# Performance work log

Hardware: AMD Instinct MI355X
Metric: run time of the kernel (lower is better)

## Reference

```python
import jax, jax.numpy as jnp
import numpy as np

B, L, H, P, S = 16, 2048, 1024, 16, 128
PAR_LEN, SENT_LEN = L // P, L // S  # 128, 16


def setup_inputs() -> dict:
    key = jax.random.key(0)
    k1, k2, k3 = jax.random.split(key, 3)
    backbone_outputs = jax.random.normal(k1, (B, L, H), dtype=jnp.float32)
    attention_mask = jnp.ones((B, L), dtype=jnp.int64)
    # structured ragged offsets: paragraph p spans [p*128, p*128+127],
    # sentence s starts at s*16 -> every paragraph contains 8 sentence heads
    par_head = jnp.tile(jnp.arange(P, dtype=jnp.int64)[None, :] * PAR_LEN, (B, 1))
    par_tail = par_head + (PAR_LEN - 1)
    sent_head = jnp.tile(jnp.arange(S, dtype=jnp.int64)[None, :] * SENT_LEN, (B, 1))
    sent_tail = sent_head + (SENT_LEN - 1)
    paragraph_attention_mask = jnp.ones((B, P), dtype=jnp.int64)
    sentence_attention_mask = jnp.ones((B, S), dtype=jnp.int64)
    # classifier params: Linear(H, 5)
    W = jax.random.normal(k2, (5, H), dtype=jnp.float32) / np.sqrt(H)
    b = jax.random.normal(k3, (5,), dtype=jnp.float32) * 0.01
    return {
        "backbone_outputs": backbone_outputs,
        "attention_mask": attention_mask,
        "paragraph_head_idxs": par_head,
        "paragraph_tail_idxs": par_tail,
        "paragraph_attention_mask": paragraph_attention_mask,
        "sentence_head_idxs": sent_head,
        "sentence_tail_idxs": sent_tail,
        "sentence_attention_mask": sentence_attention_mask,
        "W": W,
        "b": b,
    }


def reference(backbone_outputs, attention_mask, paragraph_head_idxs,
              paragraph_tail_idxs, paragraph_attention_mask,
              sentence_head_idxs, sentence_tail_idxs,
              sentence_attention_mask, W, b):
    # gather sentence-head token embeddings: [B, S, H]
    emb = jnp.take_along_axis(backbone_outputs, sentence_head_idxs[:, :, None], axis=1)
    sh = sentence_head_idxs[:, None, :]  # [B, 1, S]
    # membership: sentence head lies inside paragraph [head, tail]
    sel = (paragraph_head_idxs[:, :, None] <= sh) & (sh <= paragraph_tail_idxs[:, :, None])  # [B,P,S]
    self_f = sel.astype(emb.dtype)
    sent_cnt = jnp.maximum(self_f.sum(-1), 1.0)  # [B, P]
    # sentence -> paragraph mean (level 1)
    par_rep = jnp.einsum('bps,bsh->bph', self_f, emb) / sent_cnt[..., None]
    # paragraph skipped if tail-head<=2 or selected_head_idxs.any() is False
    par_valid = ((paragraph_tail_idxs - paragraph_head_idxs) > 2) & jnp.any(sel & (sh != 0), axis=-1)
    pv = par_valid.astype(emb.dtype)  # [B, P]
    par_cnt = jnp.maximum(pv.sum(-1), 1.0)
    # paragraph -> essay mean (level 2)
    final = jnp.einsum('bp,bph->bh', pv, par_rep) / par_cnt[:, None]
    return final @ W.T + b  # [B, 5]
```

## Files before the change

### kernel.cpp

```cpp
#include <hip/hip_runtime.h>

#define B_ 16
#define L_ 2048
#define H_ 1024
#define P_ 16
#define S_ 128

__global__ void __launch_bounds__(1024) msh_fused(
        const float* __restrict__ backbone,
        const int* __restrict__ par_head,
        const int* __restrict__ par_tail,
        const int* __restrict__ sent_head,
        const float* __restrict__ W,
        const float* __restrict__ bias,
        float* __restrict__ out) {
    int b = blockIdx.x;
    int t = threadIdx.x;

    __shared__ int   sh[S_];
    __shared__ int   ph[P_], pt[P_];
    __shared__ float inv_scnt[P_];
    __shared__ int   validp[P_];
    __shared__ float invpar;
    __shared__ float wgt[S_];
    __shared__ float red[16][5];

    if (t < S_) sh[t] = sent_head[b * S_ + t];
    if (t >= S_ && t < S_ + P_) {
        int p = t - S_;
        ph[p] = par_head[b * P_ + p];
        pt[p] = par_tail[b * P_ + p];
    }
    __syncthreads();

    {
        int p = t >> 6, lane = t & 63;
        int h0 = ph[p], t0 = pt[p];
        int s1 = lane, s2 = lane + 64;
        int in1 = (h0 <= sh[s1]) && (sh[s1] <= t0);
        int in2 = (h0 <= sh[s2]) && (sh[s2] <= t0);
        int cnt = in1 + in2;
        int nz  = (in1 && sh[s1] != 0) || (in2 && sh[s2] != 0);
        for (int off = 32; off > 0; off >>= 1) {
            cnt += __shfl_down(cnt, off, 64);
            nz  |= __shfl_down(nz,  off, 64);
        }
        if (lane == 0) {
            int valid = ((t0 - h0) > 2) && nz;
            validp[p] = valid;
            inv_scnt[p] = valid ? 1.0f / (float)(cnt > 1 ? cnt : 1) : 0.0f;
        }
    }
    __syncthreads();
    if (t == 0) {
        int pc = 0;
        for (int p = 0; p < P_; ++p) pc += validp[p];
        invpar = 1.0f / (float)(pc > 1 ? pc : 1);
    }
    __syncthreads();
    if (t < S_) {
        int myh = sh[t];
        float w = 0.0f;
        for (int p = 0; p < P_; ++p)
            if (ph[p] <= myh && myh <= pt[p]) w += inv_scnt[p];
        wgt[t] = w * invpar;
    }
    __syncthreads();

    int grp = t >> 8, q = t & 255;
    const float4* bb4 = reinterpret_cast<const float4*>(
        backbone + (size_t)b * L_ * H_);
    float4 acc = make_float4(0.f, 0.f, 0.f, 0.f);
#pragma unroll 4
    for (int s = grp; s < S_; s += 4) {
        int row = sh[s];
        float w = wgt[s];
        float4 v = bb4[row * (H_ / 4) + q];
        acc.x += w * v.x; acc.y += w * v.y; acc.z += w * v.z; acc.w += w * v.w;
    }

    const float4* W4 = reinterpret_cast<const float4*>(W);
    float pj[5];
#pragma unroll
    for (int j = 0; j < 5; ++j) {
        float4 wv = W4[j * (H_ / 4) + q];
        pj[j] = acc.x * wv.x + acc.y * wv.y + acc.z * wv.z + acc.w * wv.w;
    }
    int wave = t >> 6, lane = t & 63;
#pragma unroll
    for (int j = 0; j < 5; ++j) {
        float v = pj[j];
        for (int off = 32; off > 0; off >>= 1) v += __shfl_down(v, off, 64);
        pj[j] = v;
    }
    if (lane == 0) {
#pragma unroll
        for (int j = 0; j < 5; ++j) red[wave][j] = pj[j];
    }
    __syncthreads();

    if (t < 5) {
        float tot = 0.0f;
#pragma unroll
        for (int i = 0; i < 16; ++i) tot += red[i][t];
        out[b * 5 + t] = tot + bias[t];
    }
}

extern "C" void kernel_launch(void* const* d_in, const int* in_sizes, int n_in,
                              void* d_out, int out_size, void* d_ws, size_t ws_size,
                              hipStream_t stream) {
    const float* backbone  = (const float*)d_in[0];
    const int*   par_head  = (const int*)d_in[2];
    const int*   par_tail  = (const int*)d_in[3];
    const int*   sent_head = (const int*)d_in[5];
    const float* W         = (const float*)d_in[8];
    const float* bias      = (const float*)d_in[9];

    float* out = (float*)d_out;

    msh_fused<<<B_, 1024, 0, stream>>>(backbone, par_head, par_tail, sent_head,
                                       W, bias, out);
}
```

Baseline: 13.48 us.

## Split into weight-init kernel and wide gather kernel with atomic accumulation

The single 16-block fused kernel becomes two kernels. A small init kernel computes per-sentence weights into workspace and seeds the output with the bias. A main kernel then spreads the weighted gather and projection over 256 blocks, each covering 8 sentences, and accumulates partial results with atomicAdd. This puts far more blocks on the GPU for the memory-bound gather and skips rows whose weight is zero. The cost is a second launch, a global round trip for the weights, and float atomics that make the summation order nondeterministic.

```diff
diff --git a/kernel.cpp b/kernel.cpp
--- a/kernel.cpp
+++ b/kernel.cpp
@@ -6,49 +6,44 @@
 #define P_ 16
 #define S_ 128
 
-__global__ void __launch_bounds__(1024) msh_fused(
-        const float* __restrict__ backbone,
+__global__ void __launch_bounds__(128) msh_init(
         const int* __restrict__ par_head,
         const int* __restrict__ par_tail,
         const int* __restrict__ sent_head,
-        const float* __restrict__ W,
         const float* __restrict__ bias,
+        float* __restrict__ w_out,
         float* __restrict__ out) {
     int b = blockIdx.x;
     int t = threadIdx.x;
 
     __shared__ int   sh[S_];
-    __shared__ int   ph[P_], pt[P_];
     __shared__ float inv_scnt[P_];
     __shared__ int   validp[P_];
     __shared__ float invpar;
-    __shared__ float wgt[S_];
-    __shared__ float red[16][5];
 
-    if (t < S_) sh[t] = sent_head[b * S_ + t];
-    if (t >= S_ && t < S_ + P_) {
-        int p = t - S_;
-        ph[p] = par_head[b * P_ + p];
-        pt[p] = par_tail[b * P_ + p];
-    }
+    sh[t] = sent_head[b * S_ + t];
     __syncthreads();
 
     {
-        int p = t >> 6, lane = t & 63;
-        int h0 = ph[p], t0 = pt[p];
-        int s1 = lane, s2 = lane + 64;
-        int in1 = (h0 <= sh[s1]) && (sh[s1] <= t0);
-        int in2 = (h0 <= sh[s2]) && (sh[s2] <= t0);
-        int cnt = in1 + in2;
-        int nz  = (in1 && sh[s1] != 0) || (in2 && sh[s2] != 0);
-        for (int off = 32; off > 0; off >>= 1) {
-            cnt += __shfl_down(cnt, off, 64);
-            nz  |= __shfl_down(nz,  off, 64);
-        }
-        if (lane == 0) {
-            int valid = ((t0 - h0) > 2) && nz;
-            validp[p] = valid;
-            inv_scnt[p] = valid ? 1.0f / (float)(cnt > 1 ? cnt : 1) : 0.0f;
+        int wave = t >> 6, lane = t & 63;
+        for (int k = 0; k < 8; ++k) {
+            int p = wave * 8 + k;
+            int h0 = par_head[b * P_ + p];
+            int t0 = par_tail[b * P_ + p];
+            int s1 = lane, s2 = lane + 64;
+            int in1 = (h0 <= sh[s1]) && (sh[s1] <= t0);
+            int in2 = (h0 <= sh[s2]) && (sh[s2] <= t0);
+            int cnt = in1 + in2;
+            int nz  = (in1 && sh[s1] != 0) || (in2 && sh[s2] != 0);
+            for (int off = 32; off > 0; off >>= 1) {
+                cnt += __shfl_down(cnt, off, 64);
+                nz  |= __shfl_down(nz,  off, 64);
+            }
+            if (lane == 0) {
+                int valid = ((t0 - h0) > 2) && nz;
+                validp[p] = valid;
+                inv_scnt[p] = valid ? 1.0f / (float)(cnt > 1 ? cnt : 1) : 0.0f;
+            }
         }
     }
     __syncthreads();
@@ -58,34 +53,55 @@
         invpar = 1.0f / (float)(pc > 1 ? pc : 1);
     }
     __syncthreads();
-    if (t < S_) {
-        int myh = sh[t];
-        float w = 0.0f;
-        for (int p = 0; p < P_; ++p)
-            if (ph[p] <= myh && myh <= pt[p]) w += inv_scnt[p];
-        wgt[t] = w * invpar;
+
+    int myh = sh[t];
+    float w = 0.0f;
+    for (int p = 0; p < P_; ++p) {
+        int h0 = par_head[b * P_ + p];
+        int t0 = par_tail[b * P_ + p];
+        if (h0 <= myh && myh <= t0) w += inv_scnt[p];
     }
-    __syncthreads();
+    w_out[b * S_ + t] = w * invpar;
 
-    int grp = t >> 8, q = t & 255;
+    if (t < 5) out[b * 5 + t] = bias[t];
+}
+
+__global__ void __launch_bounds__(256) msh_main(
+        const float* __restrict__ backbone,
+        const int* __restrict__ sent_head,
+        const float* __restrict__ W,
+        const float* __restrict__ wgt,
+        float* __restrict__ out) {
+    int blk = blockIdx.x;
+    int b   = blk >> 4;
+    int sub = blk & 15;
+    int t   = threadIdx.x;
+
     const float4* bb4 = reinterpret_cast<const float4*>(
         backbone + (size_t)b * L_ * H_);
+
     float4 acc = make_float4(0.f, 0.f, 0.f, 0.f);
-#pragma unroll 4
-    for (int s = grp; s < S_; s += 4) {
-        int row = sh[s];
-        float w = wgt[s];
-        float4 v = bb4[row * (H_ / 4) + q];
-        acc.x += w * v.x; acc.y += w * v.y; acc.z += w * v.z; acc.w += w * v.w;
+    int s0 = sub * 8;
+#pragma unroll
+    for (int i = 0; i < 8; ++i) {
+        int s = s0 + i;
+        float w = wgt[b * S_ + s];
+        if (w != 0.0f) {
+            int row = sent_head[b * S_ + s];
+            float4 v = bb4[(size_t)row * (H_ / 4) + t];
+            acc.x += w * v.x; acc.y += w * v.y;
+            acc.z += w * v.z; acc.w += w * v.w;
+        }
     }
 
     const float4* W4 = reinterpret_cast<const float4*>(W);
     float pj[5];
 #pragma unroll
     for (int j = 0; j < 5; ++j) {
-        float4 wv = W4[j * (H_ / 4) + q];
+        float4 wv = W4[j * (H_ / 4) + t];
         pj[j] = acc.x * wv.x + acc.y * wv.y + acc.z * wv.z + acc.w * wv.w;
     }
+
     int wave = t >> 6, lane = t & 63;
 #pragma unroll
     for (int j = 0; j < 5; ++j) {
@@ -93,6 +109,8 @@
         for (int off = 32; off > 0; off >>= 1) v += __shfl_down(v, off, 64);
         pj[j] = v;
     }
+
+    __shared__ float red[4][5];
     if (lane == 0) {
 #pragma unroll
         for (int j = 0; j < 5; ++j) red[wave][j] = pj[j];
@@ -100,10 +118,8 @@
     __syncthreads();
 
     if (t < 5) {
-        float tot = 0.0f;
-#pragma unroll
-        for (int i = 0; i < 16; ++i) tot += red[i][t];
-        out[b * 5 + t] = tot + bias[t];
+        float tot = red[0][t] + red[1][t] + red[2][t] + red[3][t];
+        atomicAdd(out + b * 5 + t, tot);
     }
 }
 
@@ -117,8 +133,9 @@
     const float* W         = (const float*)d_in[8];
     const float* bias      = (const float*)d_in[9];
 
-    float* out = (float*)d_out;
+    float* out  = (float*)d_out;
+    float* w_ws = (float*)d_ws;
 
-    msh_fused<<<B_, 1024, 0, stream>>>(backbone, par_head, par_tail, sent_head,
-                                       W, bias, out);
+    msh_init<<<B_, 128, 0, stream>>>(par_head, par_tail, sent_head, bias, w_ws, out);
+    msh_main<<<B_ * 16, 256, 0, stream>>>(backbone, sent_head, W, w_ws, out);
 }
```

Measured after the change: 16.71 us. 1.24x slower.

## Prefetch backbone rows and W before weight computation, drop a barrier

Applied to the files above, without the earlier changes.

Issues the first eight gathered backbone row loads and the five W row loads right after the index loads, before the paragraph-weight computation. Their global-memory latency then overlaps the shared-memory weight setup. The valid-paragraph count is now computed redundantly by each of the first 128 threads, which removes one single-thread phase and one barrier. The cost is higher register pressure from holding 13 float4 values in a 1024-thread block.

```diff
diff --git a/kernel.cpp b/kernel.cpp
--- a/kernel.cpp
+++ b/kernel.cpp
@@ -16,25 +16,39 @@
         float* __restrict__ out) {
     int b = blockIdx.x;
     int t = threadIdx.x;
+    int wave = t >> 6, lane = t & 63;
+    int grp = t >> 8, q = t & 255;
 
     __shared__ int   sh[S_];
     __shared__ int   ph[P_], pt[P_];
     __shared__ float inv_scnt[P_];
     __shared__ int   validp[P_];
-    __shared__ float invpar;
     __shared__ float wgt[S_];
     __shared__ float red[16][5];
 
     if (t < S_) sh[t] = sent_head[b * S_ + t];
-    if (t >= S_ && t < S_ + P_) {
-        int p = t - S_;
-        ph[p] = par_head[b * P_ + p];
-        pt[p] = par_tail[b * P_ + p];
-    }
+    if (t < P_) { ph[t] = par_head[b * P_ + t]; pt[t] = par_tail[b * P_ + t]; }
     __syncthreads();
 
+    const float4* bb4 = reinterpret_cast<const float4*>(
+        backbone + (size_t)b * L_ * H_);
+    float4 v0 = bb4[(size_t)sh[grp +  0] * (H_/4) + q];
+    float4 v1 = bb4[(size_t)sh[grp +  4] * (H_/4) + q];
+    float4 v2 = bb4[(size_t)sh[grp +  8] * (H_/4) + q];
+    float4 v3 = bb4[(size_t)sh[grp + 12] * (H_/4) + q];
+    float4 v4 = bb4[(size_t)sh[grp + 16] * (H_/4) + q];
+    float4 v5 = bb4[(size_t)sh[grp + 20] * (H_/4) + q];
+    float4 v6 = bb4[(size_t)sh[grp + 24] * (H_/4) + q];
+    float4 v7 = bb4[(size_t)sh[grp + 28] * (H_/4) + q];
+    const float4* W4 = reinterpret_cast<const float4*>(W);
+    float4 wj0 = W4[0 * (H_/4) + q];
+    float4 wj1 = W4[1 * (H_/4) + q];
+    float4 wj2 = W4[2 * (H_/4) + q];
+    float4 wj3 = W4[3 * (H_/4) + q];
+    float4 wj4 = W4[4 * (H_/4) + q];
+
     {
-        int p = t >> 6, lane = t & 63;
+        int p  = wave;
         int h0 = ph[p], t0 = pt[p];
         int s1 = lane, s2 = lane + 64;
         int in1 = (h0 <= sh[s1]) && (sh[s1] <= t0);
@@ -52,41 +66,43 @@
         }
     }
     __syncthreads();
-    if (t == 0) {
-        int pc = 0;
-        for (int p = 0; p < P_; ++p) pc += validp[p];
-        invpar = 1.0f / (float)(pc > 1 ? pc : 1);
-    }
-    __syncthreads();
     if (t < S_) {
         int myh = sh[t];
-        float w = 0.0f;
-        for (int p = 0; p < P_; ++p)
+        float w = 0.0f; int pc = 0;
+        for (int p = 0; p < P_; ++p) {
+            pc += validp[p];
             if (ph[p] <= myh && myh <= pt[p]) w += inv_scnt[p];
-        wgt[t] = w * invpar;
+        }
+        wgt[t] = w / (float)(pc > 1 ? pc : 1);
     }
     __syncthreads();
 
-    int grp = t >> 8, q = t & 255;
-    const float4* bb4 = reinterpret_cast<const float4*>(
-        backbone + (size_t)b * L_ * H_);
     float4 acc = make_float4(0.f, 0.f, 0.f, 0.f);
-#pragma unroll 4
-    for (int s = grp; s < S_; s += 4) {
-        int row = sh[s];
+#define FMA4(wv, v) do { float _w = (wv); \
+        acc.x += _w * (v).x; acc.y += _w * (v).y; \
+        acc.z += _w * (v).z; acc.w += _w * (v).w; } while (0)
+    FMA4(wgt[grp +  0], v0);
+    FMA4(wgt[grp +  4], v1);
+    FMA4(wgt[grp +  8], v2);
+    FMA4(wgt[grp + 12], v3);
+    FMA4(wgt[grp + 16], v4);
+    FMA4(wgt[grp + 20], v5);
+    FMA4(wgt[grp + 24], v6);
+    FMA4(wgt[grp + 28], v7);
+#pragma unroll 8
+    for (int s = grp + 32; s < S_; s += 4) {
         float w = wgt[s];
-        float4 v = bb4[row * (H_ / 4) + q];
-        acc.x += w * v.x; acc.y += w * v.y; acc.z += w * v.z; acc.w += w * v.w;
+        float4 v = bb4[(size_t)sh[s] * (H_/4) + q];
+        FMA4(w, v);
     }
+#undef FMA4
 
-    const float4* W4 = reinterpret_cast<const float4*>(W);
     float pj[5];
-#pragma unroll
-    for (int j = 0; j < 5; ++j) {
-        float4 wv = W4[j * (H_ / 4) + q];
-        pj[j] = acc.x * wv.x + acc.y * wv.y + acc.z * wv.z + acc.w * wv.w;
-    }
-    int wave = t >> 6, lane = t & 63;
+    pj[0] = acc.x*wj0.x + acc.y*wj0.y + acc.z*wj0.z + acc.w*wj0.w;
+    pj[1] = acc.x*wj1.x + acc.y*wj1.y + acc.z*wj1.z + acc.w*wj1.w;
+    pj[2] = acc.x*wj2.x + acc.y*wj2.y + acc.z*wj2.z + acc.w*wj2.w;
+    pj[3] = acc.x*wj3.x + acc.y*wj3.y + acc.z*wj3.z + acc.w*wj3.w;
+    pj[4] = acc.x*wj4.x + acc.y*wj4.y + acc.z*wj4.z + acc.w*wj4.w;
 #pragma unroll
     for (int j = 0; j < 5; ++j) {
         float v = pj[j];
```

Result: faster. 12.37 us (-8.2%).

## Issue all backbone and W row loads before computing sentence weights

Applied to the files above, without the earlier changes.

All 32 gathered backbone float4 rows per thread, plus the classifier weights, are now loaded into registers right after the index loads, before the paragraph-validity and weight computation. This lets the global-memory latency overlap with the shared-memory bookkeeping instead of starting only after it. One barrier and the single-thread paragraph-count step are removed by having each weight thread count valid paragraphs itself. It needs about 150 VGPRs per thread for the preloaded data, which at 1024 threads per block risks register pressure or spilling.

```diff
diff --git a/kernel.cpp b/kernel.cpp
--- a/kernel.cpp
+++ b/kernel.cpp
@@ -16,25 +16,35 @@
         float* __restrict__ out) {
     int b = blockIdx.x;
     int t = threadIdx.x;
+    int wave = t >> 6, lane = t & 63;
+    int grp = t >> 8, q = t & 255;
 
     __shared__ int   sh[S_];
     __shared__ int   ph[P_], pt[P_];
     __shared__ float inv_scnt[P_];
     __shared__ int   validp[P_];
-    __shared__ float invpar;
     __shared__ float wgt[S_];
     __shared__ float red[16][5];
 
     if (t < S_) sh[t] = sent_head[b * S_ + t];
-    if (t >= S_ && t < S_ + P_) {
-        int p = t - S_;
-        ph[p] = par_head[b * P_ + p];
-        pt[p] = par_tail[b * P_ + p];
-    }
+    if (t < P_) { ph[t] = par_head[b * P_ + t]; pt[t] = par_tail[b * P_ + t]; }
     __syncthreads();
 
+    const float4* bb4 = reinterpret_cast<const float4*>(
+        backbone + (size_t)b * L_ * H_);
+    float4 v[32];
+#pragma unroll
+    for (int i = 0; i < 32; ++i)
+        v[i] = bb4[(size_t)sh[grp + 4 * i] * (H_ / 4) + q];
+
+    const float4* W4 = reinterpret_cast<const float4*>(W);
+    float4 wj[5];
+#pragma unroll
+    for (int j = 0; j < 5; ++j)
+        wj[j] = W4[j * (H_ / 4) + q];
+
     {
-        int p = t >> 6, lane = t & 63;
+        int p  = wave;
         int h0 = ph[p], t0 = pt[p];
         int s1 = lane, s2 = lane + 64;
         int in1 = (h0 <= sh[s1]) && (sh[s1] <= t0);
@@ -52,46 +62,35 @@
         }
     }
     __syncthreads();
-    if (t == 0) {
-        int pc = 0;
-        for (int p = 0; p < P_; ++p) pc += validp[p];
-        invpar = 1.0f / (float)(pc > 1 ? pc : 1);
-    }
-    __syncthreads();
     if (t < S_) {
         int myh = sh[t];
-        float w = 0.0f;
-        for (int p = 0; p < P_; ++p)
+        float w = 0.0f; int pc = 0;
+        for (int p = 0; p < P_; ++p) {
+            pc += validp[p];
             if (ph[p] <= myh && myh <= pt[p]) w += inv_scnt[p];
-        wgt[t] = w * invpar;
+        }
+        wgt[t] = w / (float)(pc > 1 ? pc : 1);
     }
     __syncthreads();
 
-    int grp = t >> 8, q = t & 255;
-    const float4* bb4 = reinterpret_cast<const float4*>(
-        backbone + (size_t)b * L_ * H_);
     float4 acc = make_float4(0.f, 0.f, 0.f, 0.f);
-#pragma unroll 4
-    for (int s = grp; s < S_; s += 4) {
-        int row = sh[s];
-        float w = wgt[s];
-        float4 v = bb4[row * (H_ / 4) + q];
-        acc.x += w * v.x; acc.y += w * v.y; acc.z += w * v.z; acc.w += w * v.w;
+#pragma unroll
+    for (int i = 0; i < 32; ++i) {
+        float w = wgt[grp + 4 * i];
+        acc.x += w * v[i].x; acc.y += w * v[i].y;
+        acc.z += w * v[i].z; acc.w += w * v[i].w;
     }
 
-    const float4* W4 = reinterpret_cast<const float4*>(W);
     float pj[5];
 #pragma unroll
-    for (int j = 0; j < 5; ++j) {
-        float4 wv = W4[j * (H_ / 4) + q];
-        pj[j] = acc.x * wv.x + acc.y * wv.y + acc.z * wv.z + acc.w * wv.w;
-    }
-    int wave = t >> 6, lane = t & 63;
+    for (int j = 0; j < 5; ++j)
+        pj[j] = acc.x * wj[j].x + acc.y * wj[j].y
+              + acc.z * wj[j].z + acc.w * wj[j].w;
 #pragma unroll
     for (int j = 0; j < 5; ++j) {
-        float v = pj[j];
-        for (int off = 32; off > 0; off >>= 1) v += __shfl_down(v, off, 64);
-        pj[j] = v;
+        float vv = pj[j];
+        for (int off = 32; off > 0; off >>= 1) vv += __shfl_down(vv, off, 64);
+        pj[j] = vv;
     }
     if (lane == 0) {
 #pragma unroll
```

After: 24.31 us. 1.8x slower.
